# Kernel optimization log

Hardware: AMD Instinct MI355X
Metric: run time of the kernel (lower is better)

The kernel has to match this reference:

```python
import jax, jax.numpy as jnp
import numpy as np

B, T, C = 2, 4096, 768
H = 12
D = C // H  # head_dim = 64


def setup_inputs() -> dict:
    key = jax.random.key(0)
    k1, k2, k3 = jax.random.split(key, 3)
    x = jax.random.normal(k1, (B, T, C), dtype=jnp.float32)
    Wqkv = jax.random.normal(k2, (C, 3 * C), dtype=jnp.float32) * (C ** -0.5)
    Wproj = jax.random.normal(k3, (C, C), dtype=jnp.float32) * (C ** -0.5)
    bproj = jnp.zeros((C,), dtype=jnp.float32)
    return {"x": x, "Wqkv": Wqkv, "Wproj": Wproj, "bproj": bproj}


def reference(x, Wqkv, Wproj, bproj):
    b, t, c = x.shape
    # qkv projection (no bias), split into heads: [3, B, H, T, D]
    qkv = (x @ Wqkv).reshape(b, t, 3, H, D).transpose(2, 0, 3, 1, 4)
    q, k, v = qkv[0], qkv[1], qkv[2]
    scale = D ** -0.5
    # full causal score matrix [B, H, T, T] (faithful to naive impl)
    scores = jnp.einsum('bhqd,bhkd->bhqk', q, k) * scale
    causal = jnp.tril(jnp.ones((t, t), dtype=bool))
    scores = jnp.where(causal[None, None], scores, -jnp.inf)
    attn = jax.nn.softmax(scores, axis=-1)
    out = jnp.einsum('bhqk,bhkd->bhqd', attn, v)
    out = out.transpose(0, 2, 1, 3).reshape(b, t, c)
    return out @ Wproj + bproj
```

## Files before the change

kernel.cpp:

```cpp
#include <hip/hip_runtime.h>

#define B_ 2
#define T_ 4096
#define C_ 768
#define H_ 12
#define D_ 64
#define QTASK 96

typedef __attribute__((ext_vector_type(8))) short bf16x8;
typedef __attribute__((ext_vector_type(4))) float f32x4;
typedef __attribute__((ext_vector_type(16))) float f32x16;

__device__ __forceinline__ unsigned short f2bf(float f) {
  union { float f; unsigned u; } v; v.f = f;
  unsigned r = v.u + 0x7fffu + ((v.u >> 16) & 1u);
  return (unsigned short)(r >> 16);
}

__device__ __forceinline__ float exp2_hw(float x) {
  float r;
  asm("v_exp_f32 %0, %1" : "=v"(r) : "v"(x));
  return r;
}

__device__ __forceinline__ void gll16(const void* g, void* l) {
  __builtin_amdgcn_global_load_lds((const __attribute__((address_space(1))) void*)g,
                                   (__attribute__((address_space(3))) void*)l, 16, 0, 0);
}


__global__ __launch_bounds__(256) void cast_bf16_k(const float* __restrict__ in,
                                                   unsigned short* __restrict__ out, int n4,
                                                   unsigned* __restrict__ cnt) {
  int i = blockIdx.x * 256 + threadIdx.x;
  if (i < 128) cnt[i] = 0u;
  if (i >= n4) return;
  float4 v = ((const float4*)in)[i];
  union { unsigned short s[4]; unsigned long long u; } o;
  o.s[0] = f2bf(v.x); o.s[1] = f2bf(v.y); o.s[2] = f2bf(v.z); o.s[3] = f2bf(v.w);
  ((unsigned long long*)out)[i] = o.u;
}

__global__ __launch_bounds__(256) void tpose_cast_k(const float* __restrict__ in,
                                                    unsigned short* __restrict__ out,
                                                    int R, int C) {
  __shared__ unsigned short t[64][65];
  const int c0 = blockIdx.x * 64, r0 = blockIdx.y * 64;
  const int tr = threadIdx.x >> 6, tc = threadIdx.x & 63;
#pragma unroll
  for (int i = 0; i < 16; ++i) {
    int r = i * 4 + tr;
    t[r][tc] = f2bf(in[(size_t)(r0 + r) * C + c0 + tc]);
  }
  __syncthreads();
#pragma unroll
  for (int i = 0; i < 16; ++i) {
    int c = i * 4 + tr;
    out[(size_t)(c0 + c) * R + r0 + tc] = t[tc][c];
  }
}


#define QSCALE 0.1803368801111243f

template <int MODE>
__global__ __launch_bounds__(256) void gemm_k(const unsigned short* __restrict__ A,
                                              const unsigned short* __restrict__ Bt,
                                              int K,
                                              unsigned short* __restrict__ q_out,
                                              unsigned short* __restrict__ k_out,
                                              unsigned short* __restrict__ vt_out,
                                              float* __restrict__ f_out,
                                              const float* __restrict__ bias) {
  __shared__ short a_lds[2][128 * 32];
  __shared__ short b_lds[2][128 * 32];
  const int tid = threadIdx.x;
  const int wave = tid >> 6, lane = tid & 63;
  const int wm = wave >> 1, wn = wave & 1;
  const int lr = lane & 15, lc = lane >> 4;

  const int id = blockIdx.x;
  const int xcd = id & 7, idc = id >> 3;
  const int bx = xcd * 8 + (idc & 7);
  const int by = idc >> 3;
  const int m0 = bx * 128, n0 = by * 128;

  f32x4 acc[4][4];
  for (int mi = 0; mi < 4; ++mi)
    for (int ni = 0; ni < 4; ++ni) acc[mi][ni] = (f32x4){0.f, 0.f, 0.f, 0.f};

  const unsigned short *ap[2], *bp[2];
  int lb[2];
#pragma unroll
  for (int p = 0; p < 2; ++p) {
    int chunk = p * 256 + wave * 64 + lane;
    int r = chunk >> 2, cc = chunk & 3;
    int c = cc ^ ((r >> 1) & 3);
    ap[p] = A + (size_t)(m0 + r) * K + c * 8;
    bp[p] = Bt + (size_t)(n0 + r) * K + c * 8;
    lb[p] = (p * 256 + wave * 64) * 8;
  }

  const int nks = K >> 5;
#pragma unroll
  for (int p = 0; p < 2; ++p) {
    gll16(ap[p], &a_lds[0][lb[p]]);
    gll16(bp[p], &b_lds[0][lb[p]]);
    ap[p] += 32; bp[p] += 32;
  }

  for (int ks = 0; ks < nks; ++ks) {
    const int buf = ks & 1;
    __builtin_amdgcn_s_barrier();
    __builtin_amdgcn_sched_barrier(0);
    if (ks + 1 < nks) {
#pragma unroll
      for (int p = 0; p < 2; ++p) {
        gll16(ap[p], &a_lds[buf ^ 1][lb[p]]);
        gll16(bp[p], &b_lds[buf ^ 1][lb[p]]);
        ap[p] += 32; bp[p] += 32;
      }
      asm volatile("s_waitcnt vmcnt(4)" ::: "memory");
    } else {
      asm volatile("s_waitcnt vmcnt(0)" ::: "memory");
    }
    __builtin_amdgcn_sched_barrier(0);
    __builtin_amdgcn_s_barrier();
    __builtin_amdgcn_sched_barrier(0);

    bf16x8 af[4], bfrag[4];
#pragma unroll
    for (int mi = 0; mi < 4; ++mi) {
      int r = wm * 64 + mi * 16 + lr;
      af[mi] = *(const bf16x8*)&a_lds[buf][r * 32 + (lc ^ ((r >> 1) & 3)) * 8];
    }
#pragma unroll
    for (int ni = 0; ni < 4; ++ni) {
      int r = wn * 64 + ni * 16 + lr;
      bfrag[ni] = *(const bf16x8*)&b_lds[buf][r * 32 + (lc ^ ((r >> 1) & 3)) * 8];
    }
    __builtin_amdgcn_s_setprio(1);
#pragma unroll
    for (int mi = 0; mi < 4; ++mi)
#pragma unroll
      for (int ni = 0; ni < 4; ++ni)
        acc[mi][ni] = __builtin_amdgcn_mfma_f32_16x16x32_bf16(af[mi], bfrag[ni], acc[mi][ni], 0, 0, 0);
    __builtin_amdgcn_s_setprio(0);
  }

  if (MODE == 0) {
    const int nn0 = n0 + wn * 64 + lr;
    const int which = n0 / 768;
#pragma unroll
    for (int mi = 0; mi < 4; ++mi)
#pragma unroll
      for (int ni = 0; ni < 4; ++ni) {
        int nn = nn0 + ni * 16;
        int rem = nn - which * 768;
        int h = rem >> 6, d = rem & 63;
        int t0v = m0 + wm * 64 + mi * 16 + lc * 4;
        int b = t0v >> 12, t = t0v & (T_ - 1);
        size_t bh = (size_t)(b * H_ + h);
        if (which == 2) {
          unsigned u0, u1;
          asm("v_cvt_pk_bf16_f32 %0, %1, %2" : "=v"(u0) : "v"(acc[mi][ni][0]), "v"(acc[mi][ni][1]));
          asm("v_cvt_pk_bf16_f32 %0, %1, %2" : "=v"(u1) : "v"(acc[mi][ni][2]), "v"(acc[mi][ni][3]));
          uint2 u = {u0, u1};
          *(uint2*)&vt_out[(bh * D_ + d) * T_ + t] = u;
        } else {
#pragma unroll
          for (int r = 0; r < 4; ++r) {
            float av = acc[mi][ni][r];
            if (which == 0) av *= QSCALE;
            unsigned short val = f2bf(av);
            if (which == 0) q_out[(bh * T_ + t + r) * D_ + d] = val;
            else            k_out[(bh * T_ + t + r) * D_ + d] = val;
          }
        }
      }
  } else {
#pragma unroll
    for (int mi = 0; mi < 4; ++mi)
#pragma unroll
      for (int ni = 0; ni < 4; ++ni) {
        int nn = n0 + wn * 64 + ni * 16 + lr;
        float bv = bias[nn];
#pragma unroll
        for (int r = 0; r < 4; ++r) {
          int m = m0 + wm * 64 + mi * 16 + lc * 4 + r;
          f_out[(size_t)m * C_ + nn] = acc[mi][ni][r] + bv;
        }
      }
  }
}


#define PACK8(SV, O)                                                              \
  do {                                                                            \
    unsigned w0, w1, w2, w3, w4, w5, w6, w7;                                      \
    asm("v_cvt_pk_bf16_f32 %0, %1, %2" : "=v"(w0) : "v"(SV[0]), "v"(SV[1]));      \
    asm("v_cvt_pk_bf16_f32 %0, %1, %2" : "=v"(w1) : "v"(SV[2]), "v"(SV[3]));      \
    asm("v_cvt_pk_bf16_f32 %0, %1, %2" : "=v"(w2) : "v"(SV[4]), "v"(SV[5]));      \
    asm("v_cvt_pk_bf16_f32 %0, %1, %2" : "=v"(w3) : "v"(SV[6]), "v"(SV[7]));      \
    asm("v_cvt_pk_bf16_f32 %0, %1, %2" : "=v"(w4) : "v"(SV[8]), "v"(SV[9]));      \
    asm("v_cvt_pk_bf16_f32 %0, %1, %2" : "=v"(w5) : "v"(SV[10]), "v"(SV[11]));    \
    asm("v_cvt_pk_bf16_f32 %0, %1, %2" : "=v"(w6) : "v"(SV[12]), "v"(SV[13]));    \
    asm("v_cvt_pk_bf16_f32 %0, %1, %2" : "=v"(w7) : "v"(SV[14]), "v"(SV[15]));    \
    asm("v_permlane32_swap_b32 %0, %1" : "+v"(w0), "+v"(w2));                     \
    asm("v_permlane32_swap_b32 %0, %1" : "+v"(w1), "+v"(w3));                     \
    asm("v_permlane32_swap_b32 %0, %1" : "+v"(w4), "+v"(w6));                     \
    asm("v_permlane32_swap_b32 %0, %1" : "+v"(w5), "+v"(w7));                     \
    pw[(O) + 0] = w0; pw[(O) + 1] = w1; pw[(O) + 2] = w2; pw[(O) + 3] = w3;       \
    pw[(O) + 4] = w4; pw[(O) + 5] = w5; pw[(O) + 6] = w6; pw[(O) + 7] = w7;       \
  } while (0)

__global__ __launch_bounds__(256) void flash8_k(const unsigned short* __restrict__ Qg,
                                                const unsigned short* __restrict__ Kg,
                                                const unsigned short* __restrict__ Vtg,
                                                unsigned short* __restrict__ Og,
                                                unsigned* __restrict__ cnt) {
  __shared__ short k_lds[3][8 * 512];
  __shared__ short vt_lds[3][8 * 512];
  __shared__ int task_s;

  const int tid = threadIdx.x;
  const int wave = tid >> 6, lane = tid & 63;
  const int lq = lane & 31, hi = lane >> 5;
  const int xq = blockIdx.x & 7;
  unsigned* myq = cnt + xq * 16;

  for (;;) {
    if (tid == 0) task_s = (int)atomicAdd(myq, 1u);
    __syncthreads();
    const int task = task_s;
    if (task >= QTASK) return;

    const int qi = 31 - task / 3;
    const int bh = xq * 3 + (task - (task / 3) * 3);
    const int qw = qi * 128 + wave * 32;
    const int q_g = qw + lq;

    const size_t kbase = (size_t)bh * T_ * D_;
    const size_t vbase = (size_t)bh * D_ * T_;

    const unsigned short* qrow = Qg + kbase + (size_t)q_g * D_;
    bf16x8 qf[4];
#pragma unroll
    for (int t = 0; t < 4; ++t) qf[t] = *(const bf16x8*)(qrow + t * 16 + hi * 8);

    f32x16 accT0, accT1;
#pragma unroll
    for (int r = 0; r < 16; ++r) { accT0[r] = 0.f; accT1[r] = 0.f; }
    float lvec[8];
#pragma unroll
    for (int r = 0; r < 8; ++r) lvec[r] = 0.f;
    float m = 0.f;

    const int ntl = 2 * qi + 2;

    const unsigned short* kp0 = Kg + kbase + (size_t)((wave & 1) * 32 + lq) * D_ +
                                (wave >> 1) * 16 + hi * 8;
    const unsigned short* vp0 = Vtg + vbase + (size_t)((wave & 1) * 32 + lq) * T_ +
                                (wave >> 1) * 16 + hi * 8;
    const int lb0 = wave * 512, lb1 = (wave + 4) * 512;

    auto stage = [&](int it, int sb) {
      const unsigned short* kp = kp0 + (size_t)it * 64 * D_;
      const unsigned short* vp = vp0 + it * 64;
      gll16(kp, &k_lds[sb][lb0]); gll16(kp + 32, &k_lds[sb][lb1]);
      gll16(vp, &vt_lds[sb][lb0]); gll16(vp + 32, &vt_lds[sb][lb1]);
    };

    stage(0, 0);
    stage(1, 1);

    int buf = 0;
    for (int j = 0; j < ntl; ++j) {
      const int kv = j * 64;

      __builtin_amdgcn_s_barrier();
      __builtin_amdgcn_sched_barrier(0);
      if (j + 2 < ntl) {
        int tb = buf + 2; if (tb >= 3) tb -= 3;
        stage(j + 2, tb);
        asm volatile("s_waitcnt vmcnt(8)" ::: "memory");
      } else if (j + 1 < ntl) {
        asm volatile("s_waitcnt vmcnt(4)" ::: "memory");
      } else {
        asm volatile("s_waitcnt vmcnt(0)" ::: "memory");
      }
      __builtin_amdgcn_sched_barrier(0);
      __builtin_amdgcn_s_barrier();
      __builtin_amdgcn_sched_barrier(0);

      if (kv <= qw + 31) {
        const float negm = -m;
        f32x16 s0, s1;
#pragma unroll
        for (int r = 0; r < 16; ++r) { s0[r] = negm; s1[r] = negm; }
        __builtin_amdgcn_s_setprio(1);
#pragma unroll
        for (int t = 0; t < 4; ++t) {
          bf16x8 kf0 = *(const bf16x8*)&k_lds[buf][(t * 2 + 0) * 512 + lane * 8];
          bf16x8 kf1 = *(const bf16x8*)&k_lds[buf][(t * 2 + 1) * 512 + lane * 8];
          s0 = __builtin_amdgcn_mfma_f32_32x32x16_bf16(kf0, qf[t], s0, 0, 0, 0);
          s1 = __builtin_amdgcn_mfma_f32_32x32x16_bf16(kf1, qf[t], s1, 0, 0, 0);
        }
        __builtin_amdgcn_s_setprio(0);

        if (kv + 63 > qw) {
#pragma unroll
          for (int r = 0; r < 16; ++r) {
            int key0 = kv + ((r & 3) + 8 * (r >> 2) + 4 * hi);
            if (key0 > q_g) s0[r] = -INFINITY;
            if (key0 + 32 > q_g) s1[r] = -INFINITY;
          }
        }

        float mx[16];
#pragma unroll
        for (int r = 0; r < 16; ++r) mx[r] = fmaxf(s0[r], s1[r]);
        float a0 = fmaxf(fmaxf(mx[0], mx[1]), mx[2]);
        float a1 = fmaxf(fmaxf(mx[3], mx[4]), mx[5]);
        float a2 = fmaxf(fmaxf(mx[6], mx[7]), mx[8]);
        float a3 = fmaxf(fmaxf(mx[9], mx[10]), mx[11]);
        float a4 = fmaxf(fmaxf(mx[12], mx[13]), mx[14]);
        float rx = fmaxf(fmaxf(fmaxf(a0, a1), fmaxf(a2, a3)), fmaxf(a4, mx[15]));
        rx = fmaxf(rx, __shfl_xor(rx, 32));

        if (!__all(rx <= 8.f)) {
          float dlt = fmaxf(rx, 0.f);
          float al = exp2_hw(-dlt);
          m += dlt;
#pragma unroll
          for (int r = 0; r < 16; ++r) { accT0[r] *= al; accT1[r] *= al; }
#pragma unroll
          for (int r = 0; r < 8; ++r) lvec[r] *= al;
#pragma unroll
          for (int r = 0; r < 16; ++r) { s0[r] -= dlt; s1[r] -= dlt; }
        }
#pragma unroll
        for (int r = 0; r < 16; ++r) s0[r] = exp2_hw(s0[r]);
#pragma unroll
        for (int r = 0; r < 16; ++r) s1[r] = exp2_hw(s1[r]);
#pragma unroll
        for (int r = 0; r < 8; ++r) lvec[r] += (s0[r] + s1[r]) + (s0[r + 8] + s1[r + 8]);

        unsigned pw[16];
        PACK8(s0, 0);
        PACK8(s1, 8);

        __builtin_amdgcn_s_setprio(1);
#pragma unroll
        for (int ks = 0; ks < 4; ++ks) {
          union { unsigned u[4]; bf16x8 v; } pb;
          pb.u[0] = pw[ks * 4 + 0]; pb.u[1] = pw[ks * 4 + 1];
          pb.u[2] = pw[ks * 4 + 2]; pb.u[3] = pw[ks * 4 + 3];
          bf16x8 vf0 = *(const bf16x8*)&vt_lds[buf][(ks * 2 + 0) * 512 + lane * 8];
          bf16x8 vf1 = *(const bf16x8*)&vt_lds[buf][(ks * 2 + 1) * 512 + lane * 8];
          accT0 = __builtin_amdgcn_mfma_f32_32x32x16_bf16(vf0, pb.v, accT0, 0, 0, 0);
          accT1 = __builtin_amdgcn_mfma_f32_32x32x16_bf16(vf1, pb.v, accT1, 0, 0, 0);
        }
        __builtin_amdgcn_s_setprio(0);
      }
      ++buf; if (buf >= 3) buf = 0;
    }

    float l = 0.f;
#pragma unroll
    for (int r = 0; r < 8; ++r) l += lvec[r];
    l += __shfl_xor(l, 32);
    const float inv = 1.0f / l;
    const int b = bh / H_, h = bh - b * H_;
    unsigned short* orow = Og + ((size_t)b * T_ + q_g) * C_ + h * D_;
#pragma unroll
    for (int g = 0; g < 4; ++g) {
      int d0 = 8 * g + 4 * hi;
      float e0 = accT0[4 * g + 0] * inv, e1 = accT0[4 * g + 1] * inv;
      float e2 = accT0[4 * g + 2] * inv, e3 = accT0[4 * g + 3] * inv;
      float f0 = accT1[4 * g + 0] * inv, f1 = accT1[4 * g + 1] * inv;
      float f2 = accT1[4 * g + 2] * inv, f3 = accT1[4 * g + 3] * inv;
      uint2 ua, ub;
      asm("v_cvt_pk_bf16_f32 %0, %1, %2" : "=v"(ua.x) : "v"(e0), "v"(e1));
      asm("v_cvt_pk_bf16_f32 %0, %1, %2" : "=v"(ua.y) : "v"(e2), "v"(e3));
      asm("v_cvt_pk_bf16_f32 %0, %1, %2" : "=v"(ub.x) : "v"(f0), "v"(f1));
      asm("v_cvt_pk_bf16_f32 %0, %1, %2" : "=v"(ub.y) : "v"(f2), "v"(f3));
      *(uint2*)(orow + d0) = ua;
      *(uint2*)(orow + 32 + d0) = ub;
    }
    __syncthreads();
  }
}


extern "C" void kernel_launch(void* const* d_in, const int* in_sizes, int n_in,
                              void* d_out, int out_size, void* d_ws, size_t ws_size,
                              hipStream_t stream) {
  const float* x     = (const float*)d_in[0];
  const float* Wqkv  = (const float*)d_in[1];
  const float* Wproj = (const float*)d_in[2];
  const float* bproj = (const float*)d_in[3];
  float* out = (float*)d_out;

  char* ws = (char*)d_ws;
  unsigned short* xbf   = (unsigned short*)(ws);
  unsigned short* wqkvt = (unsigned short*)(ws + 12582912);
  unsigned short* wprjt = (unsigned short*)(ws + 16121856);
  unsigned short* Qb    = (unsigned short*)(ws + 17301504);
  unsigned short* Kb    = (unsigned short*)(ws + 29884416);
  unsigned short* Vtb   = (unsigned short*)(ws + 42467328);
  unsigned*       cnt   = (unsigned*)(ws + 55050240);

  cast_bf16_k<<<6144, 256, 0, stream>>>(x, xbf, (B_ * T_ * C_) / 4, cnt);
  tpose_cast_k<<<dim3((3 * C_) / 64, C_ / 64), 256, 0, stream>>>(Wqkv, wqkvt, C_, 3 * C_);
  tpose_cast_k<<<dim3(C_ / 64, C_ / 64), 256, 0, stream>>>(Wproj, wprjt, C_, C_);

  gemm_k<0><<<(B_ * T_ / 128) * (3 * C_ / 128), 256, 0, stream>>>(
      xbf, wqkvt, C_, Qb, Kb, Vtb, nullptr, nullptr);

  flash8_k<<<512, 256, 0, stream>>>(Qb, Kb, Vtb, xbf, cnt);

  gemm_k<1><<<(B_ * T_ / 128) * (C_ / 128), 256, 0, stream>>>(
      xbf, wprjt, C_, nullptr, nullptr, nullptr, out, bproj);
}
```

Baseline: 200.6 us.

## Make flash attention waves independent with per-wave tasks and private LDS buffers

Each wave now atomically claims its own 32-query task and stages the full K and V tiles into a private LDS region, removing block-wide barriers and the shared task slot. K and V loads are split so the next K tile is prefetched after the current K fragments are read into registers, and likewise for V. This gives finer causal work balancing and no inter-wave synchronisation. In exchange, K/V global traffic per block rises because waves no longer share tiles, and pipelining is only single-buffered per stream.

```diff
diff --git a/kernel.cpp b/kernel.cpp
--- a/kernel.cpp
+++ b/kernel.cpp
@@ -5,7 +5,7 @@
 #define C_ 768
 #define H_ 12
 #define D_ 64
-#define QTASK 96
+#define WQTASK 384
 
 typedef __attribute__((ext_vector_type(8))) short bf16x8;
 typedef __attribute__((ext_vector_type(4))) float f32x4;
@@ -214,31 +214,33 @@
     pw[(O) + 4] = w4; pw[(O) + 5] = w5; pw[(O) + 6] = w6; pw[(O) + 7] = w7;       \
   } while (0)
 
-__global__ __launch_bounds__(256) void flash8_k(const unsigned short* __restrict__ Qg,
+__global__ __launch_bounds__(256) void flash9_k(const unsigned short* __restrict__ Qg,
                                                 const unsigned short* __restrict__ Kg,
                                                 const unsigned short* __restrict__ Vtg,
                                                 unsigned short* __restrict__ Og,
                                                 unsigned* __restrict__ cnt) {
-  __shared__ short k_lds[3][8 * 512];
-  __shared__ short vt_lds[3][8 * 512];
-  __shared__ int task_s;
+  __shared__ short lds[4][2][8 * 512];
 
   const int tid = threadIdx.x;
   const int wave = tid >> 6, lane = tid & 63;
   const int lq = lane & 31, hi = lane >> 5;
+  short* kbuf = &lds[wave][0][0];
+  short* vbuf = &lds[wave][1][0];
   const int xq = blockIdx.x & 7;
   unsigned* myq = cnt + xq * 16;
 
   for (;;) {
-    if (tid == 0) task_s = (int)atomicAdd(myq, 1u);
-    __syncthreads();
-    const int task = task_s;
-    if (task >= QTASK) return;
-
-    const int qi = 31 - task / 3;
-    const int bh = xq * 3 + (task - (task / 3) * 3);
-    const int qw = qi * 128 + wave * 32;
+    int t = 0;
+    if (lane == 0) t = (int)atomicAdd(myq, 1u);
+    t = __shfl(t, 0);
+    if (t >= WQTASK) return;
+
+    const int d3 = t / 3;
+    const int qs = 127 - d3;
+    const int bh = xq * 3 + (t - d3 * 3);
+    const int qw = qs * 32;
     const int q_g = qw + lq;
+    const int ntw = (qs >> 1) + 1;
 
     const size_t kbase = (size_t)bh * T_ * D_;
     const size_t vbase = (size_t)bh * D_ * T_;
@@ -246,7 +248,7 @@
     const unsigned short* qrow = Qg + kbase + (size_t)q_g * D_;
     bf16x8 qf[4];
 #pragma unroll
-    for (int t = 0; t < 4; ++t) qf[t] = *(const bf16x8*)(qrow + t * 16 + hi * 8);
+    for (int tt = 0; tt < 4; ++tt) qf[tt] = *(const bf16x8*)(qrow + tt * 16 + hi * 8);
 
     f32x16 accT0, accT1;
 #pragma unroll
@@ -256,114 +258,113 @@
     for (int r = 0; r < 8; ++r) lvec[r] = 0.f;
     float m = 0.f;
 
-    const int ntl = 2 * qi + 2;
-
-    const unsigned short* kp0 = Kg + kbase + (size_t)((wave & 1) * 32 + lq) * D_ +
-                                (wave >> 1) * 16 + hi * 8;
-    const unsigned short* vp0 = Vtg + vbase + (size_t)((wave & 1) * 32 + lq) * T_ +
-                                (wave >> 1) * 16 + hi * 8;
-    const int lb0 = wave * 512, lb1 = (wave + 4) * 512;
-
-    auto stage = [&](int it, int sb) {
-      const unsigned short* kp = kp0 + (size_t)it * 64 * D_;
-      const unsigned short* vp = vp0 + it * 64;
-      gll16(kp, &k_lds[sb][lb0]); gll16(kp + 32, &k_lds[sb][lb1]);
-      gll16(vp, &vt_lds[sb][lb0]); gll16(vp + 32, &vt_lds[sb][lb1]);
+    auto stageK = [&](int it) {
+#pragma unroll
+      for (int tt = 0; tt < 4; ++tt)
+#pragma unroll
+        for (int h = 0; h < 2; ++h)
+          gll16(Kg + kbase + (size_t)(it * 64 + h * 32 + lq) * D_ + tt * 16 + hi * 8,
+                kbuf + (tt * 2 + h) * 512);
     };
-
-    stage(0, 0);
-    stage(1, 1);
-
-    int buf = 0;
-    for (int j = 0; j < ntl; ++j) {
+    auto stageV = [&](int it) {
+#pragma unroll
+      for (int tt = 0; tt < 4; ++tt)
+#pragma unroll
+        for (int h = 0; h < 2; ++h)
+          gll16(Vtg + vbase + (size_t)(h * 32 + lq) * T_ + it * 64 + tt * 16 + hi * 8,
+                vbuf + (tt * 2 + h) * 512);
+    };
+
+    stageK(0);
+    stageV(0);
+
+    for (int j = 0; j < ntw; ++j) {
       const int kv = j * 64;
-
-      __builtin_amdgcn_s_barrier();
+      const bool pf = (j + 1 < ntw);
+
+      asm volatile("s_waitcnt vmcnt(8)" ::: "memory");
       __builtin_amdgcn_sched_barrier(0);
-      if (j + 2 < ntl) {
-        int tb = buf + 2; if (tb >= 3) tb -= 3;
-        stage(j + 2, tb);
-        asm volatile("s_waitcnt vmcnt(8)" ::: "memory");
-      } else if (j + 1 < ntl) {
-        asm volatile("s_waitcnt vmcnt(4)" ::: "memory");
-      } else {
-        asm volatile("s_waitcnt vmcnt(0)" ::: "memory");
-      }
+      bf16x8 kf[8];
+#pragma unroll
+      for (int f = 0; f < 8; ++f) kf[f] = *(const bf16x8*)&kbuf[f * 512 + lane * 8];
+      asm volatile("s_waitcnt lgkmcnt(0)" ::: "memory");
       __builtin_amdgcn_sched_barrier(0);
-      __builtin_amdgcn_s_barrier();
+      if (pf) stageK(j + 1);
+
+      const float negm = -m;
+      f32x16 s0, s1;
+#pragma unroll
+      for (int r = 0; r < 16; ++r) { s0[r] = negm; s1[r] = negm; }
+      __builtin_amdgcn_s_setprio(1);
+#pragma unroll
+      for (int tt = 0; tt < 4; ++tt) {
+        s0 = __builtin_amdgcn_mfma_f32_32x32x16_bf16(kf[2 * tt], qf[tt], s0, 0, 0, 0);
+        s1 = __builtin_amdgcn_mfma_f32_32x32x16_bf16(kf[2 * tt + 1], qf[tt], s1, 0, 0, 0);
+      }
+      __builtin_amdgcn_s_setprio(0);
+
+      if (pf) { asm volatile("s_waitcnt vmcnt(8)" ::: "memory"); }
+      else    { asm volatile("s_waitcnt vmcnt(0)" ::: "memory"); }
       __builtin_amdgcn_sched_barrier(0);
-
-      if (kv <= qw + 31) {
-        const float negm = -m;
-        f32x16 s0, s1;
-#pragma unroll
-        for (int r = 0; r < 16; ++r) { s0[r] = negm; s1[r] = negm; }
-        __builtin_amdgcn_s_setprio(1);
-#pragma unroll
-        for (int t = 0; t < 4; ++t) {
-          bf16x8 kf0 = *(const bf16x8*)&k_lds[buf][(t * 2 + 0) * 512 + lane * 8];
-          bf16x8 kf1 = *(const bf16x8*)&k_lds[buf][(t * 2 + 1) * 512 + lane * 8];
-          s0 = __builtin_amdgcn_mfma_f32_32x32x16_bf16(kf0, qf[t], s0, 0, 0, 0);
-          s1 = __builtin_amdgcn_mfma_f32_32x32x16_bf16(kf1, qf[t], s1, 0, 0, 0);
+      bf16x8 vf[8];
+#pragma unroll
+      for (int f = 0; f < 8; ++f) vf[f] = *(const bf16x8*)&vbuf[f * 512 + lane * 8];
+      asm volatile("s_waitcnt lgkmcnt(0)" ::: "memory");
+      __builtin_amdgcn_sched_barrier(0);
+      if (pf) stageV(j + 1);
+
+      if (kv + 63 > qw) {
+#pragma unroll
+        for (int r = 0; r < 16; ++r) {
+          int key0 = kv + ((r & 3) + 8 * (r >> 2) + 4 * hi);
+          if (key0 > q_g) s0[r] = -INFINITY;
+          if (key0 + 32 > q_g) s1[r] = -INFINITY;
         }
-        __builtin_amdgcn_s_setprio(0);
-
-        if (kv + 63 > qw) {
-#pragma unroll
-          for (int r = 0; r < 16; ++r) {
-            int key0 = kv + ((r & 3) + 8 * (r >> 2) + 4 * hi);
-            if (key0 > q_g) s0[r] = -INFINITY;
-            if (key0 + 32 > q_g) s1[r] = -INFINITY;
-          }
-        }
-
-        float mx[16];
-#pragma unroll
-        for (int r = 0; r < 16; ++r) mx[r] = fmaxf(s0[r], s1[r]);
-        float a0 = fmaxf(fmaxf(mx[0], mx[1]), mx[2]);
-        float a1 = fmaxf(fmaxf(mx[3], mx[4]), mx[5]);
-        float a2 = fmaxf(fmaxf(mx[6], mx[7]), mx[8]);
-        float a3 = fmaxf(fmaxf(mx[9], mx[10]), mx[11]);
-        float a4 = fmaxf(fmaxf(mx[12], mx[13]), mx[14]);
-        float rx = fmaxf(fmaxf(fmaxf(a0, a1), fmaxf(a2, a3)), fmaxf(a4, mx[15]));
-        rx = fmaxf(rx, __shfl_xor(rx, 32));
-
-        if (!__all(rx <= 8.f)) {
-          float dlt = fmaxf(rx, 0.f);
-          float al = exp2_hw(-dlt);
-          m += dlt;
-#pragma unroll
-          for (int r = 0; r < 16; ++r) { accT0[r] *= al; accT1[r] *= al; }
-#pragma unroll
-          for (int r = 0; r < 8; ++r) lvec[r] *= al;
-#pragma unroll
-          for (int r = 0; r < 16; ++r) { s0[r] -= dlt; s1[r] -= dlt; }
-        }
-#pragma unroll
-        for (int r = 0; r < 16; ++r) s0[r] = exp2_hw(s0[r]);
-#pragma unroll
-        for (int r = 0; r < 16; ++r) s1[r] = exp2_hw(s1[r]);
-#pragma unroll
-        for (int r = 0; r < 8; ++r) lvec[r] += (s0[r] + s1[r]) + (s0[r + 8] + s1[r + 8]);
-
-        unsigned pw[16];
-        PACK8(s0, 0);
-        PACK8(s1, 8);
-
-        __builtin_amdgcn_s_setprio(1);
-#pragma unroll
-        for (int ks = 0; ks < 4; ++ks) {
-          union { unsigned u[4]; bf16x8 v; } pb;
-          pb.u[0] = pw[ks * 4 + 0]; pb.u[1] = pw[ks * 4 + 1];
-          pb.u[2] = pw[ks * 4 + 2]; pb.u[3] = pw[ks * 4 + 3];
-          bf16x8 vf0 = *(const bf16x8*)&vt_lds[buf][(ks * 2 + 0) * 512 + lane * 8];
-          bf16x8 vf1 = *(const bf16x8*)&vt_lds[buf][(ks * 2 + 1) * 512 + lane * 8];
-          accT0 = __builtin_amdgcn_mfma_f32_32x32x16_bf16(vf0, pb.v, accT0, 0, 0, 0);
-          accT1 = __builtin_amdgcn_mfma_f32_32x32x16_bf16(vf1, pb.v, accT1, 0, 0, 0);
-        }
-        __builtin_amdgcn_s_setprio(0);
-      }
-      ++buf; if (buf >= 3) buf = 0;
+      }
+
+      float mx[16];
+#pragma unroll
+      for (int r = 0; r < 16; ++r) mx[r] = fmaxf(s0[r], s1[r]);
+      float a0 = fmaxf(fmaxf(mx[0], mx[1]), mx[2]);
+      float a1 = fmaxf(fmaxf(mx[3], mx[4]), mx[5]);
+      float a2 = fmaxf(fmaxf(mx[6], mx[7]), mx[8]);
+      float a3 = fmaxf(fmaxf(mx[9], mx[10]), mx[11]);
+      float a4 = fmaxf(fmaxf(mx[12], mx[13]), mx[14]);
+      float rx = fmaxf(fmaxf(fmaxf(a0, a1), fmaxf(a2, a3)), fmaxf(a4, mx[15]));
+      rx = fmaxf(rx, __shfl_xor(rx, 32));
+
+      if (!__all(rx <= 8.f)) {
+        float dlt = fmaxf(rx, 0.f);
+        float al = exp2_hw(-dlt);
+        m += dlt;
+#pragma unroll
+        for (int r = 0; r < 16; ++r) { accT0[r] *= al; accT1[r] *= al; }
+#pragma unroll
+        for (int r = 0; r < 8; ++r) lvec[r] *= al;
+#pragma unroll
+        for (int r = 0; r < 16; ++r) { s0[r] -= dlt; s1[r] -= dlt; }
+      }
+#pragma unroll
+      for (int r = 0; r < 16; ++r) s0[r] = exp2_hw(s0[r]);
+#pragma unroll
+      for (int r = 0; r < 16; ++r) s1[r] = exp2_hw(s1[r]);
+#pragma unroll
+      for (int r = 0; r < 8; ++r) lvec[r] += (s0[r] + s1[r]) + (s0[r + 8] + s1[r + 8]);
+
+      unsigned pw[16];
+      PACK8(s0, 0);
+      PACK8(s1, 8);
+
+      __builtin_amdgcn_s_setprio(1);
+#pragma unroll
+      for (int ks = 0; ks < 4; ++ks) {
+        union { unsigned u[4]; bf16x8 v; } pb;
+        pb.u[0] = pw[ks * 4 + 0]; pb.u[1] = pw[ks * 4 + 1];
+        pb.u[2] = pw[ks * 4 + 2]; pb.u[3] = pw[ks * 4 + 3];
+        accT0 = __builtin_amdgcn_mfma_f32_32x32x16_bf16(vf[2 * ks], pb.v, accT0, 0, 0, 0);
+        accT1 = __builtin_amdgcn_mfma_f32_32x32x16_bf16(vf[2 * ks + 1], pb.v, accT1, 0, 0, 0);
+      }
+      __builtin_amdgcn_s_setprio(0);
     }
 
     float l = 0.f;
@@ -388,7 +389,6 @@
       *(uint2*)(orow + d0) = ua;
       *(uint2*)(orow + 32 + d0) = ub;
     }
-    __syncthreads();
   }
 }
 
@@ -418,7 +418,7 @@
   gemm_k<0><<<(B_ * T_ / 128) * (3 * C_ / 128), 256, 0, stream>>>(
       xbf, wqkvt, C_, Qb, Kb, Vtb, nullptr, nullptr);
 
-  flash8_k<<<512, 256, 0, stream>>>(Qb, Kb, Vtb, xbf, cnt);
+  flash9_k<<<512, 256, 0, stream>>>(Qb, Kb, Vtb, xbf, cnt);
 
   gemm_k<1><<<(B_ * T_ / 128) * (C_ / 128), 256, 0, stream>>>(
       xbf, wprjt, C_, nullptr, nullptr, nullptr, out, bproj);
```

After: 294.6 us. 1.47x slower.

## Process 128-key tiles per iteration with double buffering in flash attention

Applied to the files above, without the earlier changes.

Each flash-attention loop iteration now covers 128 keys instead of 64, moving from a 3-stage ring of 64-key tiles to a 2-stage double buffer of 128-key tiles. The online-softmax max reduction and rescale are done once per 128 keys, which halves the barriers and softmax bookkeeping per key. In exchange LDS use grows, prefetch depth drops to one tile, and the partially masked second half adds branches and more live score registers, which may raise register pressure.

```diff
diff --git a/kernel.cpp b/kernel.cpp
--- a/kernel.cpp
+++ b/kernel.cpp
@@ -195,7 +195,7 @@
 }
 
 
-#define PACK8(SV, O)                                                              \
+#define PACK8(SV, PW, O)                                                          \
   do {                                                                            \
     unsigned w0, w1, w2, w3, w4, w5, w6, w7;                                      \
     asm("v_cvt_pk_bf16_f32 %0, %1, %2" : "=v"(w0) : "v"(SV[0]), "v"(SV[1]));      \
@@ -210,17 +210,17 @@
     asm("v_permlane32_swap_b32 %0, %1" : "+v"(w1), "+v"(w3));                     \
     asm("v_permlane32_swap_b32 %0, %1" : "+v"(w4), "+v"(w6));                     \
     asm("v_permlane32_swap_b32 %0, %1" : "+v"(w5), "+v"(w7));                     \
-    pw[(O) + 0] = w0; pw[(O) + 1] = w1; pw[(O) + 2] = w2; pw[(O) + 3] = w3;       \
-    pw[(O) + 4] = w4; pw[(O) + 5] = w5; pw[(O) + 6] = w6; pw[(O) + 7] = w7;       \
+    PW[(O) + 0] = w0; PW[(O) + 1] = w1; PW[(O) + 2] = w2; PW[(O) + 3] = w3;       \
+    PW[(O) + 4] = w4; PW[(O) + 5] = w5; PW[(O) + 6] = w6; PW[(O) + 7] = w7;       \
   } while (0)
 
-__global__ __launch_bounds__(256) void flash8_k(const unsigned short* __restrict__ Qg,
-                                                const unsigned short* __restrict__ Kg,
-                                                const unsigned short* __restrict__ Vtg,
-                                                unsigned short* __restrict__ Og,
-                                                unsigned* __restrict__ cnt) {
-  __shared__ short k_lds[3][8 * 512];
-  __shared__ short vt_lds[3][8 * 512];
+__global__ __launch_bounds__(256) void flash10_k(const unsigned short* __restrict__ Qg,
+                                                 const unsigned short* __restrict__ Kg,
+                                                 const unsigned short* __restrict__ Vtg,
+                                                 unsigned short* __restrict__ Og,
+                                                 unsigned* __restrict__ cnt) {
+  __shared__ short k_lds[2][16 * 512];
+  __shared__ short vt_lds[2][16 * 512];
   __shared__ int task_s;
 
   const int tid = threadIdx.x;
@@ -256,36 +256,38 @@
     for (int r = 0; r < 8; ++r) lvec[r] = 0.f;
     float m = 0.f;
 
-    const int ntl = 2 * qi + 2;
-
-    const unsigned short* kp0 = Kg + kbase + (size_t)((wave & 1) * 32 + lq) * D_ +
-                                (wave >> 1) * 16 + hi * 8;
-    const unsigned short* vp0 = Vtg + vbase + (size_t)((wave & 1) * 32 + lq) * T_ +
-                                (wave >> 1) * 16 + hi * 8;
-    const int lb0 = wave * 512, lb1 = (wave + 4) * 512;
+    const int nt = qi + 1;
+
+    const unsigned short *kb_p[4], *vb_p[4];
+    int lf[4];
+#pragma unroll
+    for (int p = 0; p < 4; ++p) {
+      int f = wave + p * 4;
+      int sub = f >> 3, tt = (f >> 1) & 3, h = f & 1;
+      kb_p[p] = Kg + kbase + (size_t)(sub * 64 + h * 32 + lq) * D_ + tt * 16 + hi * 8;
+      vb_p[p] = Vtg + vbase + (size_t)(h * 32 + lq) * T_ + sub * 64 + tt * 16 + hi * 8;
+      lf[p] = f * 512;
+    }
 
     auto stage = [&](int it, int sb) {
-      const unsigned short* kp = kp0 + (size_t)it * 64 * D_;
-      const unsigned short* vp = vp0 + it * 64;
-      gll16(kp, &k_lds[sb][lb0]); gll16(kp + 32, &k_lds[sb][lb1]);
-      gll16(vp, &vt_lds[sb][lb0]); gll16(vp + 32, &vt_lds[sb][lb1]);
+#pragma unroll
+      for (int p = 0; p < 4; ++p) {
+        gll16(kb_p[p] + (size_t)it * 128 * D_, &k_lds[sb][lf[p]]);
+        gll16(vb_p[p] + it * 128, &vt_lds[sb][lf[p]]);
+      }
     };
 
     stage(0, 0);
-    stage(1, 1);
-
-    int buf = 0;
-    for (int j = 0; j < ntl; ++j) {
-      const int kv = j * 64;
+
+    for (int j = 0; j < nt; ++j) {
+      const int kv = j * 128;
+      const int buf = j & 1;
 
       __builtin_amdgcn_s_barrier();
       __builtin_amdgcn_sched_barrier(0);
-      if (j + 2 < ntl) {
-        int tb = buf + 2; if (tb >= 3) tb -= 3;
-        stage(j + 2, tb);
+      if (j + 1 < nt) {
+        stage(j + 1, buf ^ 1);
         asm volatile("s_waitcnt vmcnt(8)" ::: "memory");
-      } else if (j + 1 < ntl) {
-        asm volatile("s_waitcnt vmcnt(4)" ::: "memory");
       } else {
         asm volatile("s_waitcnt vmcnt(0)" ::: "memory");
       }
@@ -293,77 +295,129 @@
       __builtin_amdgcn_s_barrier();
       __builtin_amdgcn_sched_barrier(0);
 
-      if (kv <= qw + 31) {
-        const float negm = -m;
-        f32x16 s0, s1;
-#pragma unroll
-        for (int r = 0; r < 16; ++r) { s0[r] = negm; s1[r] = negm; }
+      const bool act1 = (kv + 64 <= qw + 31);
+      const float negm = -m;
+
+      f32x16 s0, s1;
+#pragma unroll
+      for (int r = 0; r < 16; ++r) { s0[r] = negm; s1[r] = negm; }
+      __builtin_amdgcn_s_setprio(1);
+#pragma unroll
+      for (int t = 0; t < 4; ++t) {
+        bf16x8 kf0 = *(const bf16x8*)&k_lds[buf][(t * 2 + 0) * 512 + lane * 8];
+        bf16x8 kf1 = *(const bf16x8*)&k_lds[buf][(t * 2 + 1) * 512 + lane * 8];
+        s0 = __builtin_amdgcn_mfma_f32_32x32x16_bf16(kf0, qf[t], s0, 0, 0, 0);
+        s1 = __builtin_amdgcn_mfma_f32_32x32x16_bf16(kf1, qf[t], s1, 0, 0, 0);
+      }
+      __builtin_amdgcn_s_setprio(0);
+
+      f32x16 s2, s3;
+      if (act1) {
+#pragma unroll
+        for (int r = 0; r < 16; ++r) { s2[r] = negm; s3[r] = negm; }
         __builtin_amdgcn_s_setprio(1);
 #pragma unroll
         for (int t = 0; t < 4; ++t) {
-          bf16x8 kf0 = *(const bf16x8*)&k_lds[buf][(t * 2 + 0) * 512 + lane * 8];
-          bf16x8 kf1 = *(const bf16x8*)&k_lds[buf][(t * 2 + 1) * 512 + lane * 8];
-          s0 = __builtin_amdgcn_mfma_f32_32x32x16_bf16(kf0, qf[t], s0, 0, 0, 0);
-          s1 = __builtin_amdgcn_mfma_f32_32x32x16_bf16(kf1, qf[t], s1, 0, 0, 0);
+          bf16x8 kf0 = *(const bf16x8*)&k_lds[buf][(8 + t * 2 + 0) * 512 + lane * 8];
+          bf16x8 kf1 = *(const bf16x8*)&k_lds[buf][(8 + t * 2 + 1) * 512 + lane * 8];
+          s2 = __builtin_amdgcn_mfma_f32_32x32x16_bf16(kf0, qf[t], s2, 0, 0, 0);
+          s3 = __builtin_amdgcn_mfma_f32_32x32x16_bf16(kf1, qf[t], s3, 0, 0, 0);
         }
         __builtin_amdgcn_s_setprio(0);
-
-        if (kv + 63 > qw) {
-#pragma unroll
-          for (int r = 0; r < 16; ++r) {
-            int key0 = kv + ((r & 3) + 8 * (r >> 2) + 4 * hi);
-            if (key0 > q_g) s0[r] = -INFINITY;
-            if (key0 + 32 > q_g) s1[r] = -INFINITY;
-          }
-        }
-
-        float mx[16];
-#pragma unroll
-        for (int r = 0; r < 16; ++r) mx[r] = fmaxf(s0[r], s1[r]);
-        float a0 = fmaxf(fmaxf(mx[0], mx[1]), mx[2]);
-        float a1 = fmaxf(fmaxf(mx[3], mx[4]), mx[5]);
-        float a2 = fmaxf(fmaxf(mx[6], mx[7]), mx[8]);
-        float a3 = fmaxf(fmaxf(mx[9], mx[10]), mx[11]);
-        float a4 = fmaxf(fmaxf(mx[12], mx[13]), mx[14]);
-        float rx = fmaxf(fmaxf(fmaxf(a0, a1), fmaxf(a2, a3)), fmaxf(a4, mx[15]));
-        rx = fmaxf(rx, __shfl_xor(rx, 32));
-
-        if (!__all(rx <= 8.f)) {
-          float dlt = fmaxf(rx, 0.f);
-          float al = exp2_hw(-dlt);
-          m += dlt;
-#pragma unroll
-          for (int r = 0; r < 16; ++r) { accT0[r] *= al; accT1[r] *= al; }
-#pragma unroll
-          for (int r = 0; r < 8; ++r) lvec[r] *= al;
-#pragma unroll
-          for (int r = 0; r < 16; ++r) { s0[r] -= dlt; s1[r] -= dlt; }
-        }
-#pragma unroll
-        for (int r = 0; r < 16; ++r) s0[r] = exp2_hw(s0[r]);
-#pragma unroll
-        for (int r = 0; r < 16; ++r) s1[r] = exp2_hw(s1[r]);
-#pragma unroll
-        for (int r = 0; r < 8; ++r) lvec[r] += (s0[r] + s1[r]) + (s0[r + 8] + s1[r + 8]);
-
-        unsigned pw[16];
-        PACK8(s0, 0);
-        PACK8(s1, 8);
-
-        __builtin_amdgcn_s_setprio(1);
+      }
+
+      if (kv + 63 > qw) {
+#pragma unroll
+        for (int r = 0; r < 16; ++r) {
+          int key0 = kv + ((r & 3) + 8 * (r >> 2) + 4 * hi);
+          if (key0 > q_g) s0[r] = -INFINITY;
+          if (key0 + 32 > q_g) s1[r] = -INFINITY;
+        }
+      }
+      if (act1 && kv + 127 > qw) {
+#pragma unroll
+        for (int r = 0; r < 16; ++r) {
+          int key0 = kv + 64 + ((r & 3) + 8 * (r >> 2) + 4 * hi);
+          if (key0 > q_g) s2[r] = -INFINITY;
+          if (key0 + 32 > q_g) s3[r] = -INFINITY;
+        }
+      }
+
+      float mx[16];
+#pragma unroll
+      for (int r = 0; r < 16; ++r) mx[r] = fmaxf(s0[r], s1[r]);
+      if (act1) {
+#pragma unroll
+        for (int r = 0; r < 16; ++r) mx[r] = fmaxf(mx[r], fmaxf(s2[r], s3[r]));
+      }
+      float a0 = fmaxf(fmaxf(mx[0], mx[1]), mx[2]);
+      float a1 = fmaxf(fmaxf(mx[3], mx[4]), mx[5]);
+      float a2 = fmaxf(fmaxf(mx[6], mx[7]), mx[8]);
+      float a3 = fmaxf(fmaxf(mx[9], mx[10]), mx[11]);
+      float a4 = fmaxf(fmaxf(mx[12], mx[13]), mx[14]);
+      float rx = fmaxf(fmaxf(fmaxf(a0, a1), fmaxf(a2, a3)), fmaxf(a4, mx[15]));
+      rx = fmaxf(rx, __shfl_xor(rx, 32));
+
+      if (!__all(rx <= 8.f)) {
+        float dlt = fmaxf(rx, 0.f);
+        float al = exp2_hw(-dlt);
+        m += dlt;
+#pragma unroll
+        for (int r = 0; r < 16; ++r) { accT0[r] *= al; accT1[r] *= al; }
+#pragma unroll
+        for (int r = 0; r < 8; ++r) lvec[r] *= al;
+#pragma unroll
+        for (int r = 0; r < 16; ++r) { s0[r] -= dlt; s1[r] -= dlt; }
+        if (act1) {
+#pragma unroll
+          for (int r = 0; r < 16; ++r) { s2[r] -= dlt; s3[r] -= dlt; }
+        }
+      }
+
+#pragma unroll
+      for (int r = 0; r < 16; ++r) s0[r] = exp2_hw(s0[r]);
+#pragma unroll
+      for (int r = 0; r < 16; ++r) s1[r] = exp2_hw(s1[r]);
+#pragma unroll
+      for (int r = 0; r < 8; ++r) lvec[r] += (s0[r] + s1[r]) + (s0[r + 8] + s1[r + 8]);
+      unsigned pw0[16], pw1[16];
+      PACK8(s0, pw0, 0);
+      PACK8(s1, pw0, 8);
+      if (act1) {
+#pragma unroll
+        for (int r = 0; r < 16; ++r) s2[r] = exp2_hw(s2[r]);
+#pragma unroll
+        for (int r = 0; r < 16; ++r) s3[r] = exp2_hw(s3[r]);
+#pragma unroll
+        for (int r = 0; r < 8; ++r) lvec[r] += (s2[r] + s3[r]) + (s2[r + 8] + s3[r + 8]);
+        PACK8(s2, pw1, 0);
+        PACK8(s3, pw1, 8);
+      }
+
+      __builtin_amdgcn_s_setprio(1);
+#pragma unroll
+      for (int ks = 0; ks < 4; ++ks) {
+        union { unsigned u[4]; bf16x8 v; } pb;
+        pb.u[0] = pw0[ks * 4 + 0]; pb.u[1] = pw0[ks * 4 + 1];
+        pb.u[2] = pw0[ks * 4 + 2]; pb.u[3] = pw0[ks * 4 + 3];
+        bf16x8 vf0 = *(const bf16x8*)&vt_lds[buf][(ks * 2 + 0) * 512 + lane * 8];
+        bf16x8 vf1 = *(const bf16x8*)&vt_lds[buf][(ks * 2 + 1) * 512 + lane * 8];
+        accT0 = __builtin_amdgcn_mfma_f32_32x32x16_bf16(vf0, pb.v, accT0, 0, 0, 0);
+        accT1 = __builtin_amdgcn_mfma_f32_32x32x16_bf16(vf1, pb.v, accT1, 0, 0, 0);
+      }
+      if (act1) {
 #pragma unroll
         for (int ks = 0; ks < 4; ++ks) {
           union { unsigned u[4]; bf16x8 v; } pb;
-          pb.u[0] = pw[ks * 4 + 0]; pb.u[1] = pw[ks * 4 + 1];
-          pb.u[2] = pw[ks * 4 + 2]; pb.u[3] = pw[ks * 4 + 3];
-          bf16x8 vf0 = *(const bf16x8*)&vt_lds[buf][(ks * 2 + 0) * 512 + lane * 8];
-          bf16x8 vf1 = *(const bf16x8*)&vt_lds[buf][(ks * 2 + 1) * 512 + lane * 8];
+          pb.u[0] = pw1[ks * 4 + 0]; pb.u[1] = pw1[ks * 4 + 1];
+          pb.u[2] = pw1[ks * 4 + 2]; pb.u[3] = pw1[ks * 4 + 3];
+          bf16x8 vf0 = *(const bf16x8*)&vt_lds[buf][(8 + ks * 2 + 0) * 512 + lane * 8];
+          bf16x8 vf1 = *(const bf16x8*)&vt_lds[buf][(8 + ks * 2 + 1) * 512 + lane * 8];
           accT0 = __builtin_amdgcn_mfma_f32_32x32x16_bf16(vf0, pb.v, accT0, 0, 0, 0);
           accT1 = __builtin_amdgcn_mfma_f32_32x32x16_bf16(vf1, pb.v, accT1, 0, 0, 0);
         }
-        __builtin_amdgcn_s_setprio(0);
-      }
-      ++buf; if (buf >= 3) buf = 0;
+      }
+      __builtin_amdgcn_s_setprio(0);
     }
 
     float l = 0.f;
@@ -418,7 +472,7 @@
   gemm_k<0><<<(B_ * T_ / 128) * (3 * C_ / 128), 256, 0, stream>>>(
       xbf, wqkvt, C_, Qb, Kb, Vtb, nullptr, nullptr);
 
-  flash8_k<<<512, 256, 0, stream>>>(Qb, Kb, Vtb, xbf, cnt);
+  flash10_k<<<512, 256, 0, stream>>>(Qb, Kb, Vtb, xbf, cnt);
 
   gemm_k<1><<<(B_ * T_ / 128) * (C_ / 128), 256, 0, stream>>>(
       xbf, wprjt, C_, nullptr, nullptr, nullptr, out, bproj);
```

Result: slower. 248.9 us (+24.1%).
